# Kernel optimization log

Hardware: AMD Instinct MI355X
Metric: run time of the kernel (lower is better)

Reference implementation:

```python
import jax, jax.numpy as jnp
import numpy as np

EMBED_DIM = 768
NUM_HEADS = 12
HEAD_DIM = EMBED_DIM // NUM_HEADS


def setup_inputs() -> dict:
    key = jax.random.key(0)
    ks = jax.random.split(key, 9)
    B, S, D = 2, 2048, EMBED_DIM
    scale = 1.0 / np.sqrt(D)
    x = jax.random.normal(ks[0], (B, S, D), dtype=jnp.float32)
    Wq = jax.random.normal(ks[1], (D, D), dtype=jnp.float32) * scale
    bq = jax.random.normal(ks[2], (D,), dtype=jnp.float32) * 0.01
    Wk = jax.random.normal(ks[3], (D, D), dtype=jnp.float32) * scale
    bk = jax.random.normal(ks[4], (D,), dtype=jnp.float32) * 0.01
    Wv = jax.random.normal(ks[5], (D, D), dtype=jnp.float32) * scale
    bv = jax.random.normal(ks[6], (D,), dtype=jnp.float32) * 0.01
    Wo = jax.random.normal(ks[7], (D, D), dtype=jnp.float32) * scale
    bo = jax.random.normal(ks[8], (D,), dtype=jnp.float32) * 0.01
    return {"x": x, "Wq": Wq, "bq": bq, "Wk": Wk, "bk": bk,
            "Wv": Wv, "bv": bv, "Wo": Wo, "bo": bo}


def reference(x, Wq, bq, Wk, bk, Wv, bv, Wo, bo):
    B, S, D = x.shape
    H, Dh = NUM_HEADS, HEAD_DIM
    # separate QKV projections (weights stored [in, out] so y = x @ W + b)
    q = (x @ Wq + bq).reshape(B, S, H, Dh)
    k = (x @ Wk + bk).reshape(B, S, H, Dh)
    v = (x @ Wv + bv).reshape(B, S, H, Dh)
    # NOTE: original module applies NO 1/sqrt(head_dim) scaling
    scores = jnp.einsum('bqhd,bkhd->bhqk', q, k)          # [B,H,S,S] materialized
    attn = jax.nn.softmax(scores, axis=-1)
    ctx = jnp.einsum('bhqk,bkhd->bqhd', attn, v)          # [B,S,H,Dh]
    out = ctx.reshape(B, S, D) @ Wo + bo
    return out
```

## Files before the change

kernel.cpp:

```cpp
#include <hip/hip_runtime.h>
#include <hip/hip_bf16.h>


typedef __attribute__((ext_vector_type(8))) short short8;
typedef __attribute__((ext_vector_type(4))) float float4e;

__device__ __forceinline__ ushort f2bf(float f) {
    union { float f; unsigned u; } v; v.f = f;
    unsigned r = v.u + 0x7FFF + ((v.u >> 16) & 1);
    return (ushort)(r >> 16);
}

__device__ __forceinline__ unsigned pk2bf(float a, float b) {
    float2 t; t.x = a; t.y = b;
    __hip_bfloat162 h = __float22bfloat162_rn(t);
    union { __hip_bfloat162 h; unsigned u; } cv; cv.h = h;
    return cv.u;
}

__device__ __forceinline__ void async_cp16(const ushort* g, ushort* l) {
    __builtin_amdgcn_global_load_lds(
        (const __attribute__((address_space(1))) unsigned int*)g,
        (__attribute__((address_space(3))) unsigned int*)l,
        16, 0, 0);
}

__global__ __launch_bounds__(256) void cast_f32_bf16(
    const float* __restrict__ in, ushort* __restrict__ out, int n4)
{
    int i = blockIdx.x * blockDim.x + threadIdx.x;
    if (i < n4) {
        float4 v = *(const float4*)&in[(size_t)i * 4];
        ushort4 o;
        o.x = f2bf(v.x); o.y = f2bf(v.y); o.z = f2bf(v.z); o.w = f2bf(v.w);
        *(ushort4*)&out[(size_t)i * 4] = o;
    }
}

__global__ __launch_bounds__(256) void transpose_cast_w4(
    const float* __restrict__ W0, const float* __restrict__ W1,
    const float* __restrict__ W2, const float* __restrict__ W3,
    ushort* __restrict__ WtBase)
{
    __shared__ float t[64][65];
    const int z = blockIdx.z;
    const float* W = (z == 0) ? W0 : (z == 1) ? W1 : (z == 2) ? W2 : W3;
    ushort* Wt = WtBase + (size_t)z * (768u * 768u);

    const int tid = threadIdx.x;
    const int c  = tid & 63;
    const int rg = tid >> 6;
    const int k0 = blockIdx.y * 64, n0 = blockIdx.x * 64;
    #pragma unroll
    for (int r = 0; r < 16; ++r) {
        const int row = rg * 16 + r;
        t[row][c] = W[(size_t)(k0 + row) * 768 + n0 + c];
    }
    __syncthreads();
    #pragma unroll
    for (int r = 0; r < 16; ++r) {
        const int row = rg * 16 + r;
        Wt[(size_t)(n0 + row) * 768 + k0 + c] = f2bf(t[c][row]);
    }
}

__global__ __launch_bounds__(256) void transpose_v(
    const ushort* __restrict__ Vb, ushort* __restrict__ VT)
{
    __shared__ ushort t[64][72];
    const int tid = threadIdx.x;
    const int b = blockIdx.z, h = blockIdx.y, s0 = blockIdx.x * 64;
    const int lr = tid >> 3;
    const int lc = (tid & 7) * 8;

    #pragma unroll
    for (int half = 0; half < 64; half += 32) {
        const int row = lr + half;
        *(uint4*)&t[row][lc] =
            *(const uint4*)&Vb[(size_t)(b * 2048 + s0 + row) * 768 + h * 64 + lc];
    }
    __syncthreads();
    #pragma unroll
    for (int half = 0; half < 64; half += 32) {
        const int d = lr + half;
        ushort tmp[8];
        #pragma unroll
        for (int i = 0; i < 8; ++i) tmp[i] = t[lc + i][d];
        *(uint4*)&VT[((size_t)(b * 12 + h) * 64 + d) * 2048 + s0 + lc] =
            *(const uint4*)tmp;
    }
}

__global__ __launch_bounds__(256) void gemm_qkv_fused(
    const ushort* __restrict__ A, const ushort* __restrict__ Bt,
    const float* __restrict__ bq, const float* __restrict__ bk,
    const float* __restrict__ bv, ushort* __restrict__ Outbase)
{
    constexpr int K = 768;
    __shared__ ushort As[128][32];
    __shared__ ushort Bs[128][32];

    const int tid  = threadIdx.x;
    const int w    = tid >> 6;
    const int lane = tid & 63;
    const int l16  = lane & 15;
    const int quad = lane >> 4;
    const int wr   = (w >> 1) * 64;
    const int wc   = (w & 1) * 64;
    const int row0 = blockIdx.y * 128, col0 = blockIdx.x * 128;

    const int r4 = lane >> 2;
    const int c8 = (lane & 3) * 8;

    float4e acc[4][4];
    #pragma unroll
    for (int mi = 0; mi < 4; ++mi)
        #pragma unroll
        for (int ni = 0; ni < 4; ++ni) acc[mi][ni] = (float4e){0.f,0.f,0.f,0.f};

    for (int k0 = 0; k0 < K; k0 += 32) {
        #pragma unroll
        for (int i = 0; i < 2; ++i) {
            const int rr = w * 32 + i * 16;
            async_cp16(&A [(size_t)(row0 + rr + r4) * K + k0 + c8], &As[rr][0]);
            async_cp16(&Bt[(size_t)(col0 + rr + r4) * K + k0 + c8], &Bs[rr][0]);
        }
        __syncthreads();

        short8 af[4], bf[4];
        #pragma unroll
        for (int i = 0; i < 4; ++i) {
            af[i] = *(const short8*)&As[wr + i * 16 + l16][quad * 8];
            bf[i] = *(const short8*)&Bs[wc + i * 16 + l16][quad * 8];
        }
        #pragma unroll
        for (int mi = 0; mi < 4; ++mi)
            #pragma unroll
            for (int ni = 0; ni < 4; ++ni)
                acc[mi][ni] = __builtin_amdgcn_mfma_f32_16x16x32_bf16(
                    af[mi], bf[ni], acc[mi][ni], 0, 0, 0);
        __syncthreads();
    }

    const int seg = (col0 >= 1536) ? 2 : (col0 >= 768 ? 1 : 0);
    const float* bias = (seg == 0) ? bq : (seg == 1) ? bk : bv;
    const int ncol0 = col0 - seg * 768 + wc;
    ushort* outp = Outbase + (size_t)seg * (4096u * 768u);

    #pragma unroll
    for (int ni = 0; ni < 4; ++ni) {
        const int col = ncol0 + ni * 16 + l16;
        const float bs = bias[col];
        #pragma unroll
        for (int mi = 0; mi < 4; ++mi) {
            #pragma unroll
            for (int r = 0; r < 4; ++r) {
                const int row = row0 + wr + mi * 16 + quad * 4 + r;
                outp[(size_t)row * 768 + col] = f2bf(acc[mi][ni][r] + bs);
            }
        }
    }
}

__global__ __launch_bounds__(256) void gemm_wo_128(
    const ushort* __restrict__ A, const ushort* __restrict__ Bt,
    const float* __restrict__ bias, float* __restrict__ Cout)
{
    constexpr int K = 768, N = 768;
    __shared__ ushort As[128][40];
    __shared__ ushort Bs[128][40];

    const int tid  = threadIdx.x;
    const int w    = tid >> 6;
    const int lane = tid & 63;
    const int l16  = lane & 15;
    const int quad = lane >> 4;
    const int wr   = (w >> 1) * 64;
    const int wc   = (w & 1) * 64;
    const int row0 = blockIdx.y * 128, col0 = blockIdx.x * 128;
    const int sr = tid >> 2, sc = (tid & 3) * 8;

    float4e acc[4][4];
    #pragma unroll
    for (int mi = 0; mi < 4; ++mi)
        #pragma unroll
        for (int ni = 0; ni < 4; ++ni) acc[mi][ni] = (float4e){0.f,0.f,0.f,0.f};

    uint4 a0 = *(const uint4*)&A [(size_t)(row0 + sr     ) * K + sc];
    uint4 a1 = *(const uint4*)&A [(size_t)(row0 + sr + 64) * K + sc];
    uint4 b0 = *(const uint4*)&Bt[(size_t)(col0 + sr     ) * K + sc];
    uint4 b1 = *(const uint4*)&Bt[(size_t)(col0 + sr + 64) * K + sc];

    for (int k0 = 0; k0 < K; k0 += 32) {
        *(uint4*)&As[sr     ][sc] = a0;
        *(uint4*)&As[sr + 64][sc] = a1;
        *(uint4*)&Bs[sr     ][sc] = b0;
        *(uint4*)&Bs[sr + 64][sc] = b1;
        __syncthreads();

        if (k0 + 32 < K) {
            const int kn = k0 + 32;
            a0 = *(const uint4*)&A [(size_t)(row0 + sr     ) * K + kn + sc];
            a1 = *(const uint4*)&A [(size_t)(row0 + sr + 64) * K + kn + sc];
            b0 = *(const uint4*)&Bt[(size_t)(col0 + sr     ) * K + kn + sc];
            b1 = *(const uint4*)&Bt[(size_t)(col0 + sr + 64) * K + kn + sc];
        }

        short8 af[4], bf[4];
        #pragma unroll
        for (int i = 0; i < 4; ++i) {
            af[i] = *(const short8*)&As[wr + i * 16 + l16][quad * 8];
            bf[i] = *(const short8*)&Bs[wc + i * 16 + l16][quad * 8];
        }
        #pragma unroll
        for (int mi = 0; mi < 4; ++mi)
            #pragma unroll
            for (int ni = 0; ni < 4; ++ni)
                acc[mi][ni] = __builtin_amdgcn_mfma_f32_16x16x32_bf16(
                    af[mi], bf[ni], acc[mi][ni], 0, 0, 0);
        __syncthreads();
    }

    #pragma unroll
    for (int ni = 0; ni < 4; ++ni) {
        const int col = col0 + wc + ni * 16 + l16;
        const float bs = bias[col];
        #pragma unroll
        for (int mi = 0; mi < 4; ++mi) {
            #pragma unroll
            for (int r = 0; r < 4; ++r) {
                const int row = row0 + wr + mi * 16 + quad * 4 + r;
                Cout[(size_t)row * N + col] = acc[mi][ni][r] + bs;
            }
        }
    }
}

__global__ __launch_bounds__(512) void attn_mfma(
    const ushort* __restrict__ Qg, const ushort* __restrict__ Kgl,
    const ushort* __restrict__ VT, ushort* __restrict__ Ctx)
{
    constexpr int S = 2048, D = 768;
    __shared__ union {
        struct {
            ushort Ks [2][64][64];
            ushort Vts[2][64][64];
        } s;
        struct {
            float Osc[4][16][68];
            float Msc[4][16], Lsc[4][16];
        } c;
    } U;

    const int tid  = threadIdx.x;
    const int w    = tid >> 6;
    const int wq   = w & 3;
    const int koff = (w >> 2) * 32;
    const int lane = tid & 63;
    const int l16  = lane & 15;
    const int quad = lane >> 4;
    const int b = blockIdx.z, h = blockIdx.y, q0 = blockIdx.x * 64;
    const size_t hc = (size_t)h * 64;

    const size_t qoff = (size_t)(b * S + q0 + wq * 16 + l16) * D + hc + quad * 8;
    const short8 yq0 = *(const short8*)&Qg[qoff];
    const short8 yq1 = *(const short8*)&Qg[qoff + 32];

    const int sr  = tid >> 3;
    const int cbg = (tid & 7) ^ (sr & 7);
    const ushort* srcK = &Kgl[(size_t)(b * S + sr) * D + hc + cbg * 8];
    const ushort* srcV = &VT[((size_t)(b * 12 + h) * 64 + sr) * 2048 + cbg * 8];
    ushort* dstK0 = &U.s.Ks [0][w * 8][0];
    ushort* dstK1 = &U.s.Ks [1][w * 8][0];
    ushort* dstV0 = &U.s.Vts[0][w * 8][0];
    ushort* dstV1 = &U.s.Vts[1][w * 8][0];

    int oxk[2][2];
    #pragma unroll
    for (int kb = 0; kb < 2; ++kb) {
        const int krow = koff + kb * 16 + l16;
        oxk[kb][0] = krow * 64 + (( quad     ) ^ (krow & 7)) * 8;
        oxk[kb][1] = krow * 64 + (((quad | 4)) ^ (krow & 7)) * 8;
    }
    const int oxva = l16 * 64 + ((((koff >> 2)     + quad)) ^ ((l16 & 7) * 2)) * 4;
    const int oxvb = l16 * 64 + ((((koff >> 2) + 4 + quad)) ^ ((l16 & 7) * 2)) * 4;

    float m_ = -1e30f, l_ = 0.f;
    float4e oa[4];
    #pragma unroll
    for (int n = 0; n < 4; ++n) oa[n] = (float4e){0.f, 0.f, 0.f, 0.f};

    async_cp16(srcK, dstK0);
    async_cp16(srcV, dstV0);
    __syncthreads();

    #pragma unroll 2
    for (int k0 = 0; k0 < S; k0 += 64) {
        const int cur = (k0 >> 6) & 1;
        if (k0 + 64 < S) {
            async_cp16(srcK + (size_t)(k0 + 64) * D, cur ? dstK0 : dstK1);
            async_cp16(srcV + (k0 + 64),             cur ? dstV0 : dstV1);
        }
        const ushort* ksb = cur ? &U.s.Ks [1][0][0] : &U.s.Ks [0][0][0];
        const ushort* vsb = cur ? &U.s.Vts[1][0][0] : &U.s.Vts[0][0][0];

        float4e sa[2];
        __builtin_amdgcn_s_setprio(1);
        #pragma unroll
        for (int kb = 0; kb < 2; ++kb) {
            const short8 xk0 = *(const short8*)&ksb[oxk[kb][0]];
            const short8 xk1 = *(const short8*)&ksb[oxk[kb][1]];
            float4e z = (float4e){0.f, 0.f, 0.f, 0.f};
            z      = __builtin_amdgcn_mfma_f32_16x16x32_bf16(xk0, yq0, z, 0, 0, 0);
            sa[kb] = __builtin_amdgcn_mfma_f32_16x16x32_bf16(xk1, yq1, z, 0, 0, 0);
        }
        __builtin_amdgcn_s_setprio(0);

        float mx = -1e30f;
        #pragma unroll
        for (int kb = 0; kb < 2; ++kb)
            #pragma unroll
            for (int r = 0; r < 4; ++r) mx = fmaxf(mx, sa[kb][r]);
        mx = fmaxf(mx, __shfl_xor(mx, 16, 64));
        mx = fmaxf(mx, __shfl_xor(mx, 32, 64));

        const bool full = !__all(mx - m_ <= 8.f);
        if (full) {
            const float mn = fmaxf(m_, mx);
            const float alpha = __expf(m_ - mn);
            l_ *= alpha;
            m_ = mn;
            #pragma unroll
            for (int n = 0; n < 4; ++n)
                #pragma unroll
                for (int r = 0; r < 4; ++r) oa[n][r] *= alpha;
        }

        float p[2][4], ps = 0.f;
        #pragma unroll
        for (int kb = 0; kb < 2; ++kb)
            #pragma unroll
            for (int r = 0; r < 4; ++r) {
                p[kb][r] = __expf(sa[kb][r] - m_);
                ps += p[kb][r];
            }

        union { unsigned u[4]; short8 s8; } pa;
        pa.u[0] = pk2bf(p[0][0], p[0][1]);
        pa.u[1] = pk2bf(p[0][2], p[0][3]);
        pa.u[2] = pk2bf(p[1][0], p[1][1]);
        pa.u[3] = pk2bf(p[1][2], p[1][3]);

        ps += __shfl_xor(ps, 16, 64);
        ps += __shfl_xor(ps, 32, 64);
        l_ += ps;

        __builtin_amdgcn_s_setprio(1);
        #pragma unroll
        for (int db = 0; db < 4; ++db) {
            union { uint2 v2[2]; short8 s8; } xv;
            xv.v2[0] = *(const uint2*)&vsb[oxva + db * 1024];
            xv.v2[1] = *(const uint2*)&vsb[oxvb + db * 1024];
            oa[db] = __builtin_amdgcn_mfma_f32_16x16x32_bf16(xv.s8, pa.s8, oa[db], 0, 0, 0);
        }
        __builtin_amdgcn_s_setprio(0);

        __syncthreads();
    }

    if (w >= 4) {
        if (quad == 0) { U.c.Msc[wq][l16] = m_; U.c.Lsc[wq][l16] = l_; }
        #pragma unroll
        for (int db = 0; db < 4; ++db)
            *(float4*)&U.c.Osc[wq][l16][db * 16 + quad * 4] =
                *(const float4*)&oa[db];
    }
    __syncthreads();
    if (w < 4) {
        const float m1 = U.c.Msc[wq][l16], l1 = U.c.Lsc[wq][l16];
        const float mm = fmaxf(m_, m1);
        const float a0 = __expf(m_ - mm), a1 = __expf(m1 - mm);
        const float inv = 1.0f / (l_ * a0 + l1 * a1);
        const size_t crow = (size_t)(b * S + q0 + wq * 16 + l16) * D + hc;
        #pragma unroll
        for (int db = 0; db < 4; ++db) {
            const float4 o1 = *(const float4*)&U.c.Osc[wq][l16][db * 16 + quad * 4];
            uint2 ov;
            ov.x = pk2bf((oa[db][0] * a0 + o1.x * a1) * inv,
                         (oa[db][1] * a0 + o1.y * a1) * inv);
            ov.y = pk2bf((oa[db][2] * a0 + o1.z * a1) * inv,
                         (oa[db][3] * a0 + o1.w * a1) * inv);
            *(uint2*)&Ctx[crow + db * 16 + quad * 4] = ov;
        }
    }
}

extern "C" void kernel_launch(void* const* d_in, const int* in_sizes, int n_in,
                              void* d_out, int out_size, void* d_ws, size_t ws_size,
                              hipStream_t stream)
{
    const float* x  = (const float*)d_in[0];
    const float* Wq = (const float*)d_in[1];
    const float* bq = (const float*)d_in[2];
    const float* Wk = (const float*)d_in[3];
    const float* bk = (const float*)d_in[4];
    const float* Wv = (const float*)d_in[5];
    const float* bv = (const float*)d_in[6];
    const float* Wo = (const float*)d_in[7];
    const float* bo = (const float*)d_in[8];

    const int M = 4096, D = 768;
    const size_t XE = (size_t)M * D;
    const size_t WE = (size_t)D * D;

    ushort* xb   = (ushort*)d_ws;
    ushort* wtq  = xb   + XE;
    ushort* wto  = wtq  + 3 * WE;
    ushort* qb   = wto  + WE;
    ushort* kb   = qb   + XE;
    ushort* vb   = kb   + XE;
    ushort* ctxb = vb   + XE;
    ushort* vt   = xb;

    cast_f32_bf16<<<(int)(XE / 4 / 256), 256, 0, stream>>>(x, xb, (int)(XE / 4));

    transpose_cast_w4<<<dim3(12, 12, 4), 256, 0, stream>>>(Wq, Wk, Wv, Wo, wtq);

    gemm_qkv_fused<<<dim3(2304 / 128, 4096 / 128), 256, 0, stream>>>(
        xb, wtq, bq, bk, bv, qb);

    transpose_v<<<dim3(32, 12, 2), 256, 0, stream>>>(vb, vt);

    attn_mfma<<<dim3(2048 / 64, 12, 2), 512, 0, stream>>>(qb, kb, vt, ctxb);

    gemm_wo_128<<<dim3(768 / 128, 4096 / 128), 256, 0, stream>>>(
        ctxb, wto, bo, (float*)d_out);
}
```

Before: 191.7 us.

## Switch attention to 32x32x16 MFMA tiles with 4-way key split and 128-key blocks

Rewrites the flash-attention kernel to use 32x32x16 bf16 MFMA instructions instead of 16x16x32. The 8 waves now form 2 query groups of 32 rows times 4 key splits, and each iteration loads 128 keys instead of 64. This halves the number of loop iterations and barriers and gives fewer, larger MFMAs with less cross-lane shuffling in the softmax. The final merge now combines four partial softmax states through LDS instead of two, and the accumulators use more registers. The launch bounds now request 4 waves per EU, which may cause register spills.

```diff
diff --git a/kernel.cpp b/kernel.cpp
--- a/kernel.cpp
+++ b/kernel.cpp
@@ -4,6 +4,7 @@
 
 typedef __attribute__((ext_vector_type(8))) short short8;
 typedef __attribute__((ext_vector_type(4))) float float4e;
+typedef __attribute__((ext_vector_type(16))) float f32x16;
 
 __device__ __forceinline__ ushort f2bf(float f) {
     union { float f; unsigned u; } v; v.f = f;
@@ -236,92 +237,103 @@
     }
 }
 
-__global__ __launch_bounds__(512) void attn_mfma(
+__global__ __launch_bounds__(512, 4) void attn_mfma(
     const ushort* __restrict__ Qg, const ushort* __restrict__ Kgl,
     const ushort* __restrict__ VT, ushort* __restrict__ Ctx)
 {
     constexpr int S = 2048, D = 768;
     __shared__ union {
         struct {
-            ushort Ks [2][64][64];
-            ushort Vts[2][64][64];
+            ushort Ks [2][128][64];
+            ushort Vts[2][64][128];
         } s;
         struct {
-            float Osc[4][16][68];
-            float Msc[4][16], Lsc[4][16];
+            float Osc[6][2048];
+            float Msc[6][32];
+            float Lsc[6][32];
         } c;
     } U;
 
     const int tid  = threadIdx.x;
     const int w    = tid >> 6;
-    const int wq   = w & 3;
-    const int koff = (w >> 2) * 32;
+    const int qg   = w & 1;
+    const int ks   = w >> 1;
     const int lane = tid & 63;
-    const int l16  = lane & 15;
-    const int quad = lane >> 4;
+    const int l31  = lane & 31;
+    const int hi   = lane >> 5;
     const int b = blockIdx.z, h = blockIdx.y, q0 = blockIdx.x * 64;
     const size_t hc = (size_t)h * 64;
 
-    const size_t qoff = (size_t)(b * S + q0 + wq * 16 + l16) * D + hc + quad * 8;
-    const short8 yq0 = *(const short8*)&Qg[qoff];
-    const short8 yq1 = *(const short8*)&Qg[qoff + 32];
+    const size_t qrow = (size_t)(b * S + q0 + qg * 32 + l31) * D + hc + hi * 8;
+    short8 yq[4];
+    #pragma unroll
+    for (int dc = 0; dc < 4; ++dc) yq[dc] = *(const short8*)&Qg[qrow + dc * 16];
 
     const int sr  = tid >> 3;
-    const int cbg = (tid & 7) ^ (sr & 7);
-    const ushort* srcK = &Kgl[(size_t)(b * S + sr) * D + hc + cbg * 8];
-    const ushort* srcV = &VT[((size_t)(b * 12 + h) * 64 + sr) * 2048 + cbg * 8];
-    ushort* dstK0 = &U.s.Ks [0][w * 8][0];
-    ushort* dstK1 = &U.s.Ks [1][w * 8][0];
-    ushort* dstV0 = &U.s.Vts[0][w * 8][0];
-    ushort* dstV1 = &U.s.Vts[1][w * 8][0];
-
-    int oxk[2][2];
-    #pragma unroll
-    for (int kb = 0; kb < 2; ++kb) {
-        const int krow = koff + kb * 16 + l16;
-        oxk[kb][0] = krow * 64 + (( quad     ) ^ (krow & 7)) * 8;
-        oxk[kb][1] = krow * 64 + (((quad | 4)) ^ (krow & 7)) * 8;
-    }
-    const int oxva = l16 * 64 + ((((koff >> 2)     + quad)) ^ ((l16 & 7) * 2)) * 4;
-    const int oxvb = l16 * 64 + ((((koff >> 2) + 4 + quad)) ^ ((l16 & 7) * 2)) * 4;
+    const int kgr = (tid & 7) ^ (sr & 7);
+    const ushort* srcK = &Kgl[(size_t)(b * S + sr) * D + hc + kgr * 8];
+    const int vr  = tid >> 4;
+    const int vgr = (tid & 15) ^ (vr & 7);
+    const ushort* srcV = &VT[((size_t)(b * 12 + h) * 64 + vr) * 2048 + vgr * 8];
+    ushort* dK0 = &U.s.Ks [0][w * 8][0];
+    ushort* dK1 = &U.s.Ks [1][w * 8][0];
+    ushort* dV0 = &U.s.Vts[0][w * 4][0];
+    ushort* dV1 = &U.s.Vts[1][w * 4][0];
+
+    int okf[4];
+    #pragma unroll
+    for (int dc = 0; dc < 4; ++dc)
+        okf[dc] = (ks * 32 + l31) * 64 + ((dc * 2 + hi) ^ (l31 & 7)) * 8;
+    int ovo[2][2][2];
+    #pragma unroll
+    for (int a = 0; a < 2; ++a)
+        #pragma unroll
+        for (int m = 0; m < 2; ++m)
+            #pragma unroll
+            for (int c2 = 0; c2 < 2; ++c2)
+                ovo[a][m][c2] = (a * 32 + l31) * 128 +
+                    ((ks * 4 + m * 2 + c2) ^ (l31 & 7)) * 8 + hi * 4;
 
     float m_ = -1e30f, l_ = 0.f;
-    float4e oa[4];
-    #pragma unroll
-    for (int n = 0; n < 4; ++n) oa[n] = (float4e){0.f, 0.f, 0.f, 0.f};
-
-    async_cp16(srcK, dstK0);
-    async_cp16(srcV, dstV0);
+    f32x16 oa0, oa1;
+    #pragma unroll
+    for (int i = 0; i < 16; ++i) { oa0[i] = 0.f; oa1[i] = 0.f; }
+
+    async_cp16(srcK,                  dK0);
+    async_cp16(srcK + (size_t)64 * D, dK0 + 64 * 64);
+    async_cp16(srcV,                  dV0);
+    async_cp16(srcV + 32 * 2048,      dV0 + 32 * 128);
     __syncthreads();
 
     #pragma unroll 2
-    for (int k0 = 0; k0 < S; k0 += 64) {
-        const int cur = (k0 >> 6) & 1;
-        if (k0 + 64 < S) {
-            async_cp16(srcK + (size_t)(k0 + 64) * D, cur ? dstK0 : dstK1);
-            async_cp16(srcV + (k0 + 64),             cur ? dstV0 : dstV1);
-        }
+    for (int t = 0; t < 16; ++t) {
+        const int cur = t & 1;
         const ushort* ksb = cur ? &U.s.Ks [1][0][0] : &U.s.Ks [0][0][0];
         const ushort* vsb = cur ? &U.s.Vts[1][0][0] : &U.s.Vts[0][0][0];
-
-        float4e sa[2];
+        if (t + 1 < 16) {
+            const size_t kn = (size_t)(t + 1) * 128;
+            ushort* dK = cur ? dK0 : dK1;
+            ushort* dV = cur ? dV0 : dV1;
+            async_cp16(srcK + kn * D,              dK);
+            async_cp16(srcK + (kn + 64) * D,       dK + 64 * 64);
+            async_cp16(srcV + kn,                  dV);
+            async_cp16(srcV + kn + 32 * 2048,      dV + 32 * 128);
+        }
+
+        f32x16 sa;
+        #pragma unroll
+        for (int i = 0; i < 16; ++i) sa[i] = 0.f;
         __builtin_amdgcn_s_setprio(1);
         #pragma unroll
-        for (int kb = 0; kb < 2; ++kb) {
-            const short8 xk0 = *(const short8*)&ksb[oxk[kb][0]];
-            const short8 xk1 = *(const short8*)&ksb[oxk[kb][1]];
-            float4e z = (float4e){0.f, 0.f, 0.f, 0.f};
-            z      = __builtin_amdgcn_mfma_f32_16x16x32_bf16(xk0, yq0, z, 0, 0, 0);
-            sa[kb] = __builtin_amdgcn_mfma_f32_16x16x32_bf16(xk1, yq1, z, 0, 0, 0);
+        for (int dc = 0; dc < 4; ++dc) {
+            const short8 xk = *(const short8*)&ksb[okf[dc]];
+            sa = __builtin_amdgcn_mfma_f32_32x32x16_bf16(xk, yq[dc], sa, 0, 0, 0);
         }
         __builtin_amdgcn_s_setprio(0);
 
-        float mx = -1e30f;
-        #pragma unroll
-        for (int kb = 0; kb < 2; ++kb)
-            #pragma unroll
-            for (int r = 0; r < 4; ++r) mx = fmaxf(mx, sa[kb][r]);
-        mx = fmaxf(mx, __shfl_xor(mx, 16, 64));
+        float mx = sa[0];
+        #pragma unroll
+        for (int r = 1; r < 16; ++r) mx = fmaxf(mx, sa[r]);
         mx = fmaxf(mx, __shfl_xor(mx, 32, 64));
 
         const bool full = !__all(mx - m_ <= 8.f);
@@ -331,67 +343,104 @@
             l_ *= alpha;
             m_ = mn;
             #pragma unroll
-            for (int n = 0; n < 4; ++n)
-                #pragma unroll
-                for (int r = 0; r < 4; ++r) oa[n][r] *= alpha;
-        }
-
-        float p[2][4], ps = 0.f;
-        #pragma unroll
-        for (int kb = 0; kb < 2; ++kb)
-            #pragma unroll
-            for (int r = 0; r < 4; ++r) {
-                p[kb][r] = __expf(sa[kb][r] - m_);
-                ps += p[kb][r];
-            }
-
-        union { unsigned u[4]; short8 s8; } pa;
-        pa.u[0] = pk2bf(p[0][0], p[0][1]);
-        pa.u[1] = pk2bf(p[0][2], p[0][3]);
-        pa.u[2] = pk2bf(p[1][0], p[1][1]);
-        pa.u[3] = pk2bf(p[1][2], p[1][3]);
-
-        ps += __shfl_xor(ps, 16, 64);
+            for (int i = 0; i < 16; ++i) { oa0[i] *= alpha; oa1[i] *= alpha; }
+        }
+
+        float p[16], ps = 0.f;
+        #pragma unroll
+        for (int r = 0; r < 16; ++r) {
+            p[r] = __expf(sa[r] - m_);
+            ps += p[r];
+        }
         ps += __shfl_xor(ps, 32, 64);
         l_ += ps;
 
+        union { unsigned u[4]; short8 s8; } pa0, pa1;
+        pa0.u[0] = pk2bf(p[0],  p[1]);  pa0.u[1] = pk2bf(p[2],  p[3]);
+        pa0.u[2] = pk2bf(p[4],  p[5]);  pa0.u[3] = pk2bf(p[6],  p[7]);
+        pa1.u[0] = pk2bf(p[8],  p[9]);  pa1.u[1] = pk2bf(p[10], p[11]);
+        pa1.u[2] = pk2bf(p[12], p[13]); pa1.u[3] = pk2bf(p[14], p[15]);
+
         __builtin_amdgcn_s_setprio(1);
-        #pragma unroll
-        for (int db = 0; db < 4; ++db) {
+        {
             union { uint2 v2[2]; short8 s8; } xv;
-            xv.v2[0] = *(const uint2*)&vsb[oxva + db * 1024];
-            xv.v2[1] = *(const uint2*)&vsb[oxvb + db * 1024];
-            oa[db] = __builtin_amdgcn_mfma_f32_16x16x32_bf16(xv.s8, pa.s8, oa[db], 0, 0, 0);
+            xv.v2[0] = *(const uint2*)&vsb[ovo[0][0][0]];
+            xv.v2[1] = *(const uint2*)&vsb[ovo[0][0][1]];
+            oa0 = __builtin_amdgcn_mfma_f32_32x32x16_bf16(xv.s8, pa0.s8, oa0, 0, 0, 0);
+            xv.v2[0] = *(const uint2*)&vsb[ovo[0][1][0]];
+            xv.v2[1] = *(const uint2*)&vsb[ovo[0][1][1]];
+            oa0 = __builtin_amdgcn_mfma_f32_32x32x16_bf16(xv.s8, pa1.s8, oa0, 0, 0, 0);
+            xv.v2[0] = *(const uint2*)&vsb[ovo[1][0][0]];
+            xv.v2[1] = *(const uint2*)&vsb[ovo[1][0][1]];
+            oa1 = __builtin_amdgcn_mfma_f32_32x32x16_bf16(xv.s8, pa0.s8, oa1, 0, 0, 0);
+            xv.v2[0] = *(const uint2*)&vsb[ovo[1][1][0]];
+            xv.v2[1] = *(const uint2*)&vsb[ovo[1][1][1]];
+            oa1 = __builtin_amdgcn_mfma_f32_32x32x16_bf16(xv.s8, pa1.s8, oa1, 0, 0, 0);
         }
         __builtin_amdgcn_s_setprio(0);
 
         __syncthreads();
     }
 
-    if (w >= 4) {
-        if (quad == 0) { U.c.Msc[wq][l16] = m_; U.c.Lsc[wq][l16] = l_; }
-        #pragma unroll
-        for (int db = 0; db < 4; ++db)
-            *(float4*)&U.c.Osc[wq][l16][db * 16 + quad * 4] =
-                *(const float4*)&oa[db];
+    if (ks > 0) {
+        const int slot = (ks - 1) * 2 + qg;
+        float* ob = &U.c.Osc[slot][lane * 32];
+        #pragma unroll
+        for (int g = 0; g < 4; ++g) {
+            float4 v0, v1;
+            v0.x = oa0[g * 4 + 0]; v0.y = oa0[g * 4 + 1];
+            v0.z = oa0[g * 4 + 2]; v0.w = oa0[g * 4 + 3];
+            v1.x = oa1[g * 4 + 0]; v1.y = oa1[g * 4 + 1];
+            v1.z = oa1[g * 4 + 2]; v1.w = oa1[g * 4 + 3];
+            *(float4*)&ob[(( g     ) ^ (lane & 7)) * 4] = v0;
+            *(float4*)&ob[(((g + 4)) ^ (lane & 7)) * 4] = v1;
+        }
+        if (hi == 0) {
+            U.c.Msc[slot][l31] = m_;
+            U.c.Lsc[slot][l31] = l_;
+        }
     }
     __syncthreads();
-    if (w < 4) {
-        const float m1 = U.c.Msc[wq][l16], l1 = U.c.Lsc[wq][l16];
-        const float mm = fmaxf(m_, m1);
-        const float a0 = __expf(m_ - mm), a1 = __expf(m1 - mm);
-        const float inv = 1.0f / (l_ * a0 + l1 * a1);
-        const size_t crow = (size_t)(b * S + q0 + wq * 16 + l16) * D + hc;
-        #pragma unroll
-        for (int db = 0; db < 4; ++db) {
-            const float4 o1 = *(const float4*)&U.c.Osc[wq][l16][db * 16 + quad * 4];
-            uint2 ov;
-            ov.x = pk2bf((oa[db][0] * a0 + o1.x * a1) * inv,
-                         (oa[db][1] * a0 + o1.y * a1) * inv);
-            ov.y = pk2bf((oa[db][2] * a0 + o1.z * a1) * inv,
-                         (oa[db][3] * a0 + o1.w * a1) * inv);
-            *(uint2*)&Ctx[crow + db * 16 + quad * 4] = ov;
-        }
+    if (ks == 0) {
+        const float m1 = U.c.Msc[qg][l31];
+        const float m2 = U.c.Msc[2 + qg][l31];
+        const float m3 = U.c.Msc[4 + qg][l31];
+        const float M  = fmaxf(fmaxf(m_, m1), fmaxf(m2, m3));
+        const float a0 = __expf(m_ - M), a1 = __expf(m1 - M),
+                    a2 = __expf(m2 - M), a3 = __expf(m3 - M);
+        const float l1 = U.c.Lsc[qg][l31];
+        const float l2 = U.c.Lsc[2 + qg][l31];
+        const float l3 = U.c.Lsc[4 + qg][l31];
+        const float inv = 1.0f / (l_ * a0 + l1 * a1 + l2 * a2 + l3 * a3);
+
+        float o[32];
+        #pragma unroll
+        for (int i = 0; i < 16; ++i) { o[i] = oa0[i] * a0; o[16 + i] = oa1[i] * a0; }
+        #pragma unroll
+        for (int s = 0; s < 3; ++s) {
+            const float as = (s == 0) ? a1 : (s == 1) ? a2 : a3;
+            const float* ob = &U.c.Osc[s * 2 + qg][lane * 32];
+            #pragma unroll
+            for (int gg = 0; gg < 8; ++gg) {
+                const float4 v = *(const float4*)&ob[(gg ^ (lane & 7)) * 4];
+                o[gg * 4 + 0] += v.x * as;
+                o[gg * 4 + 1] += v.y * as;
+                o[gg * 4 + 2] += v.z * as;
+                o[gg * 4 + 3] += v.w * as;
+            }
+        }
+
+        const size_t crow = (size_t)(b * S + q0 + qg * 32 + l31) * D + hc;
+        #pragma unroll
+        for (int a = 0; a < 2; ++a)
+            #pragma unroll
+            for (int rq = 0; rq < 4; ++rq) {
+                const int base = a * 16 + rq * 4;
+                uint2 ov;
+                ov.x = pk2bf(o[base + 0] * inv, o[base + 1] * inv);
+                ov.y = pk2bf(o[base + 2] * inv, o[base + 3] * inv);
+                *(uint2*)&Ctx[crow + a * 32 + rq * 8 + hi * 4] = ov;
+            }
     }
 }
 
```

New measurement: 183.1 us. -4.5%, faster.
